# Kernel tuning notes

Measured on AMD Instinct MI355X. Metric: run time of the kernel, lower is better.

## Reference

```python
import jax, jax.numpy as jnp
import numpy as np

T, B = 8192, 4096
NEG_SLOPE = 0.01


def setup_inputs() -> dict:
    key = jax.random.key(0)
    k1, k2 = jax.random.split(key)
    input_seq = jax.random.randint(k1, (T, B), 0, 2, dtype=jnp.int32)
    delta = jax.random.normal(k2, (2,), dtype=jnp.float32)
    return {"input_seq": input_seq, "delta": delta}


def reference(input_seq, delta):
    # Per-step: counter += delta[inp]; output = leaky_relu(counter).
    # counter itself is never clamped, so this is exactly
    # leaky_relu(cumsum(delta[input_seq], axis=time)).
    steps = delta[input_seq]                 # [T, B] gather from 2-entry table
    counter = jnp.cumsum(steps, axis=0)      # [T, B] prefix sum over time
    return jnp.where(counter >= 0, counter, NEG_SLOPE * counter)
```

## Files before the change

### kernel.cpp

```cpp
#include <hip/hip_runtime.h>
#include <stdint.h>

#define T_DIM 8192
#define B_DIM 4096
#define NSEG 64
#define CTILE 256
#define NEG_SLOPE 0.01f

typedef int      ivec4 __attribute__((ext_vector_type(4)));
typedef float    fvec4 __attribute__((ext_vector_type(4)));
typedef unsigned uvec4 __attribute__((ext_vector_type(4)));


__global__ __launch_bounds__(256, 4) void ka_pack(const int* __restrict__ in,
                                                  uint32_t* __restrict__ bits,
                                                  int* __restrict__ segTotal) {
    const int c4 = threadIdx.x & 63;
    const int rc = threadIdx.x >> 6;
    const int col0 = blockIdx.x * CTILE + c4 * 4;
    const int wordrow = blockIdx.y * 4 + rc;
    const int row0 = wordrow * 32;

    const ivec4* __restrict__ inv = (const ivec4*)in;
    uint32_t b0 = 0, b1 = 0, b2 = 0, b3 = 0;
#pragma unroll
    for (int r = 0; r < 32; ++r) {
        ivec4 v = __builtin_nontemporal_load(&inv[((size_t)(row0 + r) * B_DIM + col0) >> 2]);
        b0 |= ((uint32_t)v.x & 1u) << r;
        b1 |= ((uint32_t)v.y & 1u) << r;
        b2 |= ((uint32_t)v.z & 1u) << r;
        b3 |= ((uint32_t)v.w & 1u) << r;
    }

    ((uint4*)bits)[((size_t)wordrow * B_DIM + col0) >> 2] = make_uint4(b0, b1, b2, b3);

    __shared__ int4 cnts[4][64];
    cnts[rc][c4] = make_int4(__popc(b0), __popc(b1), __popc(b2), __popc(b3));
    __syncthreads();

    if (rc == 0) {
        int4 s = cnts[0][c4];
#pragma unroll
        for (int i = 1; i < 4; ++i) {
            int4 v = cnts[i][c4];
            s.x += v.x; s.y += v.y; s.z += v.z; s.w += v.w;
        }
        ((int4*)segTotal)[((size_t)blockIdx.y * B_DIM + col0) >> 2] = s;
    }
}

__global__ __launch_bounds__(256, 4) void kb_emit(const uint32_t* __restrict__ bits,
                                                  const int* __restrict__ segTotal,
                                                  const float* __restrict__ delta,
                                                  float* __restrict__ out) {
    const int c4 = threadIdx.x & 63;
    const int rc = threadIdx.x >> 6;
    const int col0 = blockIdx.x * CTILE + c4 * 4;
    const int seg = blockIdx.y;
    const int wordrow = seg * 4 + rc;
    const int row0 = wordrow * 32;

    uvec4 w = __builtin_nontemporal_load(
        &((const uvec4*)bits)[((size_t)wordrow * B_DIM + col0) >> 2]);

    __shared__ int4 cnts[4][64];
    cnts[rc][c4] = make_int4(__popc(w.x), __popc(w.y), __popc(w.z), __popc(w.w));

    int c0 = 0, c1 = 0, c2 = 0, c3 = 0;
    for (int s = 0; s < seg; ++s) {
        int4 v = ((const int4*)segTotal)[((size_t)s * B_DIM + col0) >> 2];
        c0 += v.x; c1 += v.y; c2 += v.z; c3 += v.w;
    }
    __syncthreads();

    for (int i = 0; i < rc; ++i) {
        int4 v = cnts[i][c4];
        c0 += v.x; c1 += v.y; c2 += v.z; c3 += v.w;
    }

    const float d0 = delta[0];
    const float dd = delta[1] - d0;

    fvec4* __restrict__ outv = (fvec4*)out;
#pragma unroll
    for (int r = 0; r < 32; ++r) {
        const int t = row0 + r;
        const float tp = (float)(t + 1) * d0;
        c0 += (int)((w.x >> r) & 1u);
        c1 += (int)((w.y >> r) & 1u);
        c2 += (int)((w.z >> r) & 1u);
        c3 += (int)((w.w >> r) & 1u);
        fvec4 o;
        float ox = fmaf((float)c0, dd, tp);
        float oy = fmaf((float)c1, dd, tp);
        float oz = fmaf((float)c2, dd, tp);
        float ow = fmaf((float)c3, dd, tp);
        o.x = (ox >= 0.0f) ? ox : NEG_SLOPE * ox;
        o.y = (oy >= 0.0f) ? oy : NEG_SLOPE * oy;
        o.z = (oz >= 0.0f) ? oz : NEG_SLOPE * oz;
        o.w = (ow >= 0.0f) ? ow : NEG_SLOPE * ow;
        __builtin_nontemporal_store(o, &outv[((size_t)t * B_DIM + col0) >> 2]);
    }
}

extern "C" void kernel_launch(void* const* d_in, const int* in_sizes, int n_in,
                              void* d_out, int out_size, void* d_ws, size_t ws_size,
                              hipStream_t stream) {
    const int*   in    = (const int*)d_in[0];
    const float* delta = (const float*)d_in[1];
    float*       out   = (float*)d_out;

    uint32_t* bits     = (uint32_t*)d_ws;
    int*      segTotal = (int*)((char*)d_ws + (size_t)(T_DIM / 32) * B_DIM * 4);

    dim3 grid(B_DIM / CTILE, NSEG);
    dim3 block(256);

    hipLaunchKernelGGL(ka_pack, grid, block, 0, stream, in, bits, segTotal);
    hipLaunchKernelGGL(kb_emit, grid, block, 0, stream, bits, segTotal, delta, out);
}
```

Before: 224.3 us.

## Fuse pack and emit into single-pass scan with ticketed decoupled lookback

Replaces the two-kernel pack-then-emit pipeline with one kernel. Each block takes a dynamic ticket to pick its segment and stripe, publishes its per-column segment totals as packed 16-bit counts (offset by one so zero means not ready) via atomic stores, and spins on predecessor segments' aggregates to build its prefix. This drops the bit-packed intermediate's write and re-read and one kernel launch. In exchange it adds a memset of the workspace, spin-wait latency along the segment chain, and an O(seg) aggregate read per block.

```diff
diff --git a/kernel.cpp b/kernel.cpp
--- a/kernel.cpp
+++ b/kernel.cpp
@@ -4,22 +4,37 @@
 #define T_DIM 8192
 #define B_DIM 4096
 #define NSEG 64
+#define NSTRIPE 16
 #define CTILE 256
 #define NEG_SLOPE 0.01f
 
 typedef int      ivec4 __attribute__((ext_vector_type(4)));
 typedef float    fvec4 __attribute__((ext_vector_type(4)));
-typedef unsigned uvec4 __attribute__((ext_vector_type(4)));
 
 
-__global__ __launch_bounds__(256, 4) void ka_pack(const int* __restrict__ in,
-                                                  uint32_t* __restrict__ bits,
-                                                  int* __restrict__ segTotal) {
-    const int c4 = threadIdx.x & 63;
-    const int rc = threadIdx.x >> 6;
-    const int col0 = blockIdx.x * CTILE + c4 * 4;
-    const int wordrow = blockIdx.y * 4 + rc;
-    const int row0 = wordrow * 32;
+__global__ __launch_bounds__(256, 4) void fused_scan(
+        const int*   __restrict__ in,
+        const float* __restrict__ delta,
+        float*       __restrict__ out,
+        unsigned long long* __restrict__ agg,
+        int*         __restrict__ ticket)
+{
+    __shared__ int  s_tick;
+    __shared__ int4 cnts[4][64];
+    __shared__ int4 part[4][64];
+
+    if (threadIdx.x == 0) s_tick = atomicAdd(ticket, 1);
+    __syncthreads();
+    const int tick   = s_tick;
+    const int stripe = tick & (NSTRIPE - 1);
+    const int seg    = tick >> 4;
+
+    const int c4      = threadIdx.x & 63;
+    const int rc      = threadIdx.x >> 6;
+    const int col0    = stripe * CTILE + c4 * 4;
+    const int wordrow = seg * 4 + rc;
+    const int row0    = wordrow * 32;
+    const int cq      = col0 >> 2;
 
     const ivec4* __restrict__ inv = (const ivec4*)in;
     uint32_t b0 = 0, b1 = 0, b2 = 0, b3 = 0;
@@ -31,10 +46,6 @@
         b2 |= ((uint32_t)v.z & 1u) << r;
         b3 |= ((uint32_t)v.w & 1u) << r;
     }
-
-    ((uint4*)bits)[((size_t)wordrow * B_DIM + col0) >> 2] = make_uint4(b0, b1, b2, b3);
-
-    __shared__ int4 cnts[4][64];
     cnts[rc][c4] = make_int4(__popc(b0), __popc(b1), __popc(b2), __popc(b3));
     __syncthreads();
 
@@ -45,34 +56,38 @@
             int4 v = cnts[i][c4];
             s.x += v.x; s.y += v.y; s.z += v.z; s.w += v.w;
         }
-        ((int4*)segTotal)[((size_t)blockIdx.y * B_DIM + col0) >> 2] = s;
+        unsigned long long val =
+              (unsigned long long)(unsigned)(s.x + 1)
+            | ((unsigned long long)(unsigned)(s.y + 1) << 16)
+            | ((unsigned long long)(unsigned)(s.z + 1) << 32)
+            | ((unsigned long long)(unsigned)(s.w + 1) << 48);
+        __hip_atomic_store(&agg[(size_t)seg * (B_DIM / 4) + cq], val,
+                           __ATOMIC_RELAXED, __HIP_MEMORY_SCOPE_AGENT);
     }
-}
-
-__global__ __launch_bounds__(256, 4) void kb_emit(const uint32_t* __restrict__ bits,
-                                                  const int* __restrict__ segTotal,
-                                                  const float* __restrict__ delta,
-                                                  float* __restrict__ out) {
-    const int c4 = threadIdx.x & 63;
-    const int rc = threadIdx.x >> 6;
-    const int col0 = blockIdx.x * CTILE + c4 * 4;
-    const int seg = blockIdx.y;
-    const int wordrow = seg * 4 + rc;
-    const int row0 = wordrow * 32;
-
-    uvec4 w = __builtin_nontemporal_load(
-        &((const uvec4*)bits)[((size_t)wordrow * B_DIM + col0) >> 2]);
-
-    __shared__ int4 cnts[4][64];
-    cnts[rc][c4] = make_int4(__popc(w.x), __popc(w.y), __popc(w.z), __popc(w.w));
 
     int c0 = 0, c1 = 0, c2 = 0, c3 = 0;
-    for (int s = 0; s < seg; ++s) {
-        int4 v = ((const int4*)segTotal)[((size_t)s * B_DIM + col0) >> 2];
+    for (int s = rc; s < seg; s += 4) {
+        unsigned long long v = __hip_atomic_load(&agg[(size_t)s * (B_DIM / 4) + cq],
+                                                 __ATOMIC_RELAXED, __HIP_MEMORY_SCOPE_AGENT);
+        while ((v & 0xFFFFull) == 0ull) {
+            __builtin_amdgcn_s_sleep(1);
+            v = __hip_atomic_load(&agg[(size_t)s * (B_DIM / 4) + cq],
+                                  __ATOMIC_RELAXED, __HIP_MEMORY_SCOPE_AGENT);
+        }
+        c0 += (int)( v        & 0xFFFF) - 1;
+        c1 += (int)((v >> 16) & 0xFFFF) - 1;
+        c2 += (int)((v >> 32) & 0xFFFF) - 1;
+        c3 += (int)((v >> 48) & 0xFFFF) - 1;
+    }
+    part[rc][c4] = make_int4(c0, c1, c2, c3);
+    __syncthreads();
+
+    c0 = 0; c1 = 0; c2 = 0; c3 = 0;
+#pragma unroll
+    for (int i = 0; i < 4; ++i) {
+        int4 v = part[i][c4];
         c0 += v.x; c1 += v.y; c2 += v.z; c3 += v.w;
     }
-    __syncthreads();
-
     for (int i = 0; i < rc; ++i) {
         int4 v = cnts[i][c4];
         c0 += v.x; c1 += v.y; c2 += v.z; c3 += v.w;
@@ -86,10 +101,10 @@
     for (int r = 0; r < 32; ++r) {
         const int t = row0 + r;
         const float tp = (float)(t + 1) * d0;
-        c0 += (int)((w.x >> r) & 1u);
-        c1 += (int)((w.y >> r) & 1u);
-        c2 += (int)((w.z >> r) & 1u);
-        c3 += (int)((w.w >> r) & 1u);
+        c0 += (int)((b0 >> r) & 1u);
+        c1 += (int)((b1 >> r) & 1u);
+        c2 += (int)((b2 >> r) & 1u);
+        c3 += (int)((b3 >> r) & 1u);
         fvec4 o;
         float ox = fmaf((float)c0, dd, tp);
         float oy = fmaf((float)c1, dd, tp);
@@ -110,12 +125,12 @@
     const float* delta = (const float*)d_in[1];
     float*       out   = (float*)d_out;
 
-    uint32_t* bits     = (uint32_t*)d_ws;
-    int*      segTotal = (int*)((char*)d_ws + (size_t)(T_DIM / 32) * B_DIM * 4);
+    unsigned long long* agg = (unsigned long long*)d_ws;
+    const size_t agg_bytes  = (size_t)NSEG * (B_DIM / 4) * sizeof(unsigned long long);
+    int* ticket = (int*)((char*)d_ws + agg_bytes);
 
-    dim3 grid(B_DIM / CTILE, NSEG);
-    dim3 block(256);
+    hipMemsetAsync(d_ws, 0, agg_bytes + 64, stream);
 
-    hipLaunchKernelGGL(ka_pack, grid, block, 0, stream, in, bits, segTotal);
-    hipLaunchKernelGGL(kb_emit, grid, block, 0, stream, bits, segTotal, delta, out);
+    hipLaunchKernelGGL(fused_scan, dim3(1024), dim3(256), 0, stream,
+                       in, delta, out, agg, ticket);
 }
```

Result: slower. 284.1 us (+26.7%).
